# Optimization experiments

Measured on AMD Instinct MI355X. Metric: run time of the kernel, lower is better.

Reference implementation:

```python
import jax, jax.numpy as jnp
import numpy as np

H = 200   # hidden_size
P = 4     # maxout_pool_size
T = 4     # max_dec_steps
B = 64
M = 1000
NEG = -1e30


def setup_inputs():
    key = jax.random.key(0)
    ks = jax.random.split(key, 20)
    def rn(k, shape, scale=0.05):
        return jax.random.normal(k, shape, dtype=jnp.float32) * scale
    inp = {}
    inp["U"] = jax.random.normal(ks[0], (B, M, 2 * H), dtype=jnp.float32)
    inp["d_mask"] = jnp.ones((B, M), dtype=jnp.int32)
    inp["span"] = jax.random.randint(ks[1], (B, 2), 0, M)
    # LSTM: input 4H, hidden H, 1 layer, torch forget-gate bias init (f gate = 1)
    inp["w_ih"] = rn(ks[2], (4 * H, 4 * H))
    inp["w_hh"] = rn(ks[3], (4 * H, H))
    inp["b_ih"] = jnp.zeros((4 * H,), jnp.float32).at[H:2 * H].set(1.0)
    inp["b_hh"] = jnp.zeros((4 * H,), jnp.float32)
    # two HighwayMaxout heads (start 's', end 'e')
    for tag, off in (("s", 4), ("e", 11)):
        inp[f"Wr_{tag}"] = rn(ks[off + 0], (H, 5 * H))          # linear, no bias
        inp[f"W1_{tag}"] = rn(ks[off + 1], (H * P, 3 * H))
        inp[f"b1_{tag}"] = jnp.zeros((H * P,), jnp.float32)
        inp[f"W2_{tag}"] = rn(ks[off + 2], (H * P, H))
        inp[f"b2_{tag}"] = jnp.zeros((H * P,), jnp.float32)
        inp[f"W12_{tag}"] = rn(ks[off + 3], (P, 2 * H))
        inp[f"b12_{tag}"] = jnp.zeros((P,), jnp.float32)
    return inp


def lstm_step(x, h, c, w_ih, w_hh, b_ih, b_hh):
    # torch gate order: i, f, g, o
    g = x @ w_ih.T + h @ w_hh.T + b_ih + b_hh
    i, f, gg, o = jnp.split(g, 4, axis=-1)
    c = jax.nn.sigmoid(f) * c + jax.nn.sigmoid(i) * jnp.tanh(gg)
    h = jax.nn.sigmoid(o) * jnp.tanh(c)
    return h, c


def hmn(h, U, u_cat, mask_mult, Wr, W1, b1, W2, b2, W12, b12):
    b, m, _ = U.shape
    r = jnp.tanh(jnp.concatenate([h, u_cat], 1) @ Wr.T)                      # (b,H)
    x = jnp.concatenate([U, jnp.broadcast_to(r[:, None, :], (b, m, H))], 2)  # (b,m,3H)
    m1 = (x @ W1.T + b1).reshape(b, m, H, P).max(-1)                          # (b,m,H)
    m2 = (m1 @ W2.T + b2).reshape(b, m, H, P).max(-1)                         # (b,m,H)
    alpha = (jnp.concatenate([m1, m2], 2) @ W12.T + b12).max(-1)             # (b,m)
    return jax.nn.log_softmax(alpha + mask_mult, axis=1)


def reference(U, d_mask, span, w_ih, w_hh, b_ih, b_hh,
              Wr_s, W1_s, b1_s, W2_s, b2_s, W12_s, b12_s,
              Wr_e, W1_e, b1_e, W2_e, b2_e, W12_e, b12_e):
    b, m, _ = U.shape
    bidx = jnp.arange(b)
    mask_mult = (1.0 - d_mask.astype(jnp.float32)) * NEG
    s_tgt = span[:, 0]
    e_tgt = span[:, 1]
    ps = (Wr_s, W1_s, b1_s, W2_s, b2_s, W12_s, b12_s)
    pe = (Wr_e, W1_e, b1_e, W2_e, b2_e, W12_e, b12_e)

    s0 = jnp.zeros((b,), jnp.int32)
    e0 = (jnp.sum(d_mask, 1) - 1).astype(jnp.int32)
    u_s0 = U[bidx, s0]
    h0 = jnp.zeros((b, H), U.dtype)
    c0 = jnp.zeros((b, H), U.dtype)
    m0 = jnp.ones((b,), bool)

    def step(carry, first):
        s, e, u_s, h, c, ms, me = carry
        u_e = U[bidx, e]
        u_cat = jnp.concatenate([u_s, u_e], 1)               # (b,4H)
        h, c = lstm_step(u_cat, h, c, w_ih, w_hh, b_ih, b_hh)
        # start head
        a_s = hmn(h, U, u_cat, mask_mult, *ps)
        idx_s = jnp.argmax(a_s, 1).astype(jnp.int32)
        s_new = jnp.where(first, idx_s, idx_s * ms)
        ms_new = jnp.where(first, True, s_new != s * ms)
        ls = -jnp.mean(jnp.take_along_axis(a_s, s_tgt[:, None], 1)) * ms_new.astype(U.dtype)
        # end head (u_s refreshed with new start)
        u_s2 = U[bidx, s_new]
        u_cat2 = jnp.concatenate([u_s2, u_e], 1)
        a_e = hmn(h, U, u_cat2, mask_mult, *pe)
        idx_e = jnp.argmax(a_e, 1).astype(jnp.int32)
        e_new = jnp.where(first, idx_e, idx_e * me)
        me_new = jnp.where(first, True, e_new != e * me)
        le = -jnp.mean(jnp.take_along_axis(a_e, e_tgt[:, None], 1)) * me_new.astype(U.dtype)
        return (s_new, e_new, u_s2, h, c, ms_new, me_new), (s_new, ms_new, e_new, me_new, ls + le)

    firsts = jnp.arange(T) == 0
    _, (ss, mss, es, mes, losses) = jax.lax.scan(step, (s0, e0, u_s0, h0, c0, m0, m0), firsts)

    pos_s = jnp.sum(mss.astype(jnp.int32), 0) - 1            # (b,)
    p1 = ss[pos_s, bidx]
    pos_e = jnp.sum(mes.astype(jnp.int32), 0) - 1
    p2 = es[pos_e, bidx]
    loss = jnp.mean(jnp.sum(losses, 0)) / T
    return loss, p1, p2
```

## Files before the change

### kernel.cpp

```cpp
#include <hip/hip_runtime.h>
#include <math.h>

#define H 200
#define TT 4
#define BB 64
#define MM 1000
#define NEGV (-1e30f)

static const int ROWS = BB * MM;
#define KA 416
#define KB 224
#define NPAD 896
#define NSLICE 28
#define LSTR 40
#define RP 500
#define GG 3528

typedef __attribute__((ext_vector_type(8))) short short8;
typedef __attribute__((ext_vector_type(4))) float f32x4;

__device__ __forceinline__ void split2(float x, unsigned short& h, unsigned short& l) {
  unsigned u = __float_as_uint(x);
  h = (unsigned short)(u >> 16);
  float res = x - __uint_as_float(u & 0xffff0000u);
  l = (unsigned short)(__float_as_uint(res) >> 16);
}
__device__ __forceinline__ float bf2f(unsigned short h) {
  return __uint_as_float(((unsigned)h) << 16);
}
__device__ __forceinline__ void gload16(const unsigned short* g, const unsigned short* l) {
  __builtin_amdgcn_global_load_lds(
      (const __attribute__((address_space(1))) void*)g,
      (__attribute__((address_space(3))) void*)l, 16, 0, 0);
}

__global__ __launch_bounds__(256) void k_init(const int* __restrict__ dmask,
    int* st_s, int* st_e, int* ms, int* me,
    float* h, float* c, float* out) {
  int b = blockIdx.x, t = threadIdx.x;
  __shared__ int red[256];
  int sum = 0;
  for (int m = t; m < MM; m += 256) sum += dmask[b * MM + m];
  red[t] = sum; __syncthreads();
  for (int s = 128; s > 0; s >>= 1) { if (t < s) red[t] += red[t + s]; __syncthreads(); }
  if (t == 0) { st_s[b] = 0; st_e[b] = red[0] - 1; ms[b] = 1; me[b] = 1; }
  for (int i = t; i < H; i += 256) { h[b * H + i] = 0.f; c[b * H + i] = 0.f; }
  if (b == 0 && t == 0) out[0] = 0.f;
}

__global__ __launch_bounds__(256) void k_T(const float* __restrict__ src, int ld,
    int R, int koff, float* __restrict__ dst) {
  int k = blockIdx.x;
  for (int r = threadIdx.x; r < R; r += 256)
    dst[(size_t)k * R + r] = src[(size_t)r * ld + koff + k];
}

__global__ __launch_bounds__(256) void k_splitP(const float* __restrict__ src, int srcld,
    int Ksrc, int Nsrc,
    unsigned short* __restrict__ hi, unsigned short* __restrict__ lo, int Kpad) {
  int r = blockIdx.x;
  int r7 = r & 127;
  size_t pbase = (size_t)(r >> 7) * (size_t)(128 * Kpad);
  int sw = (r7 >> 1) & 3;
  for (int k = threadIdx.x; k < Kpad; k += 256) {
    unsigned short h = 0, l = 0;
    if (r < Nsrc && k < Ksrc) split2(src[(size_t)r * srcld + k], h, l);
    size_t addr = pbase + (size_t)(k >> 5) * 4096 + r7 * 32 +
                  ((((k >> 3) & 3) ^ sw) << 3) + (k & 7);
    hi[addr] = h; lo[addr] = l;
  }
}

__global__ __launch_bounds__(256) void k_splitPW1(const float* __restrict__ src,
    unsigned short* __restrict__ hi, unsigned short* __restrict__ lo) {
  int r = blockIdx.x;
  int o = (r & ~63) + ((r & 15) << 2) + ((r >> 4) & 3);
  int r7 = r & 127;
  size_t pbase = (size_t)(r >> 7) * (size_t)(128 * KA);
  int sw = (r7 >> 1) & 3;
  for (int k = threadIdx.x; k < KA; k += 256) {
    unsigned short h = 0, l = 0;
    if (o < 800 && k < 400) split2(src[(size_t)o * 600 + k], h, l);
    size_t addr = pbase + (size_t)(k >> 5) * 4096 + r7 * 32 +
                  ((((k >> 3) & 3) ^ sw) << 3) + (k & 7);
    hi[addr] = h; lo[addr] = l;
  }
}

__global__ __launch_bounds__(256) void k_split(const float* __restrict__ src, int srcld,
    int Ksrc, int Nsrc,
    unsigned short* __restrict__ hi, unsigned short* __restrict__ lo, int Kpad) {
  int r = blockIdx.x;
  for (int k = threadIdx.x; k < Kpad; k += 256) {
    unsigned short h = 0, l = 0;
    if (r < Nsrc && k < Ksrc) split2(src[(size_t)r * srcld + k], h, l);
    hi[(size_t)r * Kpad + k] = h;
    lo[(size_t)r * Kpad + k] = l;
  }
}

__global__ __launch_bounds__(256) void k_prep(const float* __restrict__ U,
    const int* __restrict__ st_s, const int* __restrict__ st_e,
    float* __restrict__ ucat, float* __restrict__ ue) {
  int b = blockIdx.x, t = threadIdx.x;
  int si = st_s[b], ei = st_e[b];
  const float* Us = U + ((size_t)b * MM + si) * 400;
  const float* Ue = U + ((size_t)b * MM + ei) * 400;
  for (int i = t; i < 400; i += 256) {
    float uv = Ue[i];
    ucat[b * 800 + i] = Us[i];
    ucat[b * 800 + 400 + i] = uv;
    ue[b * 400 + i] = uv;
  }
}

__global__ __launch_bounds__(256) void k_gates(
    const float* __restrict__ ucat, const float* __restrict__ hbuf,
    const float* __restrict__ wTih, const float* __restrict__ wThh,
    const float* __restrict__ b_ih, const float* __restrict__ b_hh,
    float* __restrict__ g) {
  const int b = blockIdx.y, t = threadIdx.x;
  const int o = blockIdx.x * 64 + (t & 63);
  const int oc = o < 800 ? o : 799;
  const int ks = t >> 6;
  __shared__ float xs[800], hs[200], red[256];
  for (int i = t; i < 800; i += 256) xs[i] = ucat[b * 800 + i];
  for (int i = t; i < 200; i += 256) hs[i] = hbuf[b * H + i];
  __syncthreads();
  float acc = 0.f;
#pragma unroll 8
  for (int k = ks * 200; k < ks * 200 + 200; ++k)
    acc = fmaf(wTih[(size_t)k * 800 + oc], xs[k], acc);
#pragma unroll 8
  for (int k = ks * 50; k < ks * 50 + 50; ++k)
    acc = fmaf(wThh[(size_t)k * 800 + oc], hs[k], acc);
  red[t] = acc; __syncthreads();
  if (ks == 0 && o < 800)
    g[b * 800 + o] = red[t] + red[t + 64] + red[t + 128] + red[t + 192] + b_ih[o] + b_hh[o];
}

__global__ __launch_bounds__(256) void k_act(const float* __restrict__ g,
    float* __restrict__ h, float* __restrict__ c) {
  int b = blockIdx.x, t = threadIdx.x;
  if (t >= H) return;
  float ig = 1.f / (1.f + expf(-g[b * 800 + t]));
  float fg = 1.f / (1.f + expf(-g[b * 800 + 200 + t]));
  float gg = tanhf(g[b * 800 + 400 + t]);
  float og = 1.f / (1.f + expf(-g[b * 800 + 600 + t]));
  float cn = fg * c[b * H + t] + ig * gg;
  c[b * H + t] = cn;
  h[b * H + t] = og * tanhf(cn);
}

template <int TAG>
__global__ __launch_bounds__(256) void k_r2(
    const float* __restrict__ U, const int* __restrict__ st_s,
    const float* __restrict__ ucat, const float* __restrict__ ue,
    const float* __restrict__ hbuf, const float* __restrict__ WrT,
    float* __restrict__ rbuf) {
  const int b = blockIdx.y, t = threadIdx.x;
  const int o = blockIdx.x * 64 + (t & 63);
  const int oc = o < 200 ? o : 199;
  const int ks = t >> 6;
  __shared__ float xcs[1000], red[256];
  for (int i = t; i < 200; i += 256) xcs[i] = hbuf[b * H + i];
  if (TAG == 0) {
    for (int i = t; i < 800; i += 256) xcs[200 + i] = ucat[b * 800 + i];
  } else {
    const float* Us = U + ((size_t)b * MM + st_s[b]) * 400;
    for (int i = t; i < 400; i += 256) {
      xcs[200 + i] = Us[i];
      xcs[600 + i] = ue[b * 400 + i];
    }
  }
  __syncthreads();
  float acc = 0.f;
#pragma unroll 8
  for (int k = ks * 250; k < ks * 250 + 250; ++k)
    acc = fmaf(WrT[(size_t)k * 200 + oc], xcs[k], acc);
  red[t] = acc; __syncthreads();
  if (ks == 0 && o < 200)
    rbuf[b * 200 + o] = tanhf(red[t] + red[t + 64] + red[t + 128] + red[t + 192]);
}

__global__ __launch_bounds__(256) void k_rcorr(
    const float* __restrict__ rbuf, const float* __restrict__ W1cT,
    const float* __restrict__ b1, float* __restrict__ rcorr) {
  const int b = blockIdx.y, t = threadIdx.x;
  const int o = blockIdx.x * 64 + (t & 63);
  const int oc = o < 800 ? o : 799;
  const int ks = t >> 6;
  __shared__ float rs[200], red[256];
  for (int i = t; i < 200; i += 256) rs[i] = rbuf[b * 200 + i];
  __syncthreads();
  float acc = 0.f;
#pragma unroll 8
  for (int k = ks * 50; k < ks * 50 + 50; ++k)
    acc = fmaf(W1cT[(size_t)k * 800 + oc], rs[k], acc);
  red[t] = acc; __syncthreads();
  if (ks == 0)
    rcorr[b * NPAD + o] = (o < 800)
        ? red[t] + red[t + 64] + red[t + 128] + red[t + 192] + b1[o] : 0.f;
}

__global__ __launch_bounds__(1024) void k_lstm_r(
    const float* __restrict__ U, const int* __restrict__ st_s, const int* __restrict__ st_e,
    float* __restrict__ h, float* __restrict__ c,
    const float* __restrict__ w_ih, const float* __restrict__ w_hh,
    const float* __restrict__ b_ih, const float* __restrict__ b_hh,
    const float* __restrict__ Wr, const float* __restrict__ W1, const float* __restrict__ b1,
    float* __restrict__ rcorr, float* __restrict__ ue) {
  int b = blockIdx.x, t = threadIdx.x;
  __shared__ float xc[1000];
  __shared__ float hold[H];
  __shared__ float g[800];
  __shared__ float r[H];
  int si = st_s[b], ei = st_e[b];
  const float* Us = U + ((size_t)b * MM + si) * 400;
  const float* Ue = U + ((size_t)b * MM + ei) * 400;
  if (t < 400) { xc[200 + t] = Us[t]; xc[600 + t] = Ue[t]; ue[b * 400 + t] = Ue[t]; }
  if (t >= 400 && t < 600) hold[t - 400] = h[b * H + (t - 400)];
  __syncthreads();
  if (t < 800) {
    float acc = b_ih[t] + b_hh[t];
    const float4* wi = (const float4*)(w_ih + (size_t)t * 800);
    const float* xv = &xc[200];
    for (int k = 0; k < 200; ++k) {
      float4 wv = wi[k];
      acc = fmaf(wv.x, xv[k * 4 + 0], acc); acc = fmaf(wv.y, xv[k * 4 + 1], acc);
      acc = fmaf(wv.z, xv[k * 4 + 2], acc); acc = fmaf(wv.w, xv[k * 4 + 3], acc);
    }
    const float4* wh = (const float4*)(w_hh + (size_t)t * H);
    for (int k = 0; k < 50; ++k) {
      float4 wv = wh[k];
      acc = fmaf(wv.x, hold[k * 4 + 0], acc); acc = fmaf(wv.y, hold[k * 4 + 1], acc);
      acc = fmaf(wv.z, hold[k * 4 + 2], acc); acc = fmaf(wv.w, hold[k * 4 + 3], acc);
    }
    g[t] = acc;
  }
  __syncthreads();
  if (t < H) {
    float ig = 1.f / (1.f + expf(-g[t]));
    float fg = 1.f / (1.f + expf(-g[H + t]));
    float gg = tanhf(g[2 * H + t]);
    float og = 1.f / (1.f + expf(-g[3 * H + t]));
    float cn = fg * c[b * H + t] + ig * gg;
    c[b * H + t] = cn;
    float hv = og * tanhf(cn);
    h[b * H + t] = hv;
    xc[t] = hv;
  }
  __syncthreads();
  if (t < H) {
    float acc = 0.f;
    const float4* wr = (const float4*)(Wr + (size_t)t * 1000);
    for (int k = 0; k < 250; ++k) {
      float4 wv = wr[k];
      acc = fmaf(wv.x, xc[k * 4 + 0], acc); acc = fmaf(wv.y, xc[k * 4 + 1], acc);
      acc = fmaf(wv.z, xc[k * 4 + 2], acc); acc = fmaf(wv.w, xc[k * 4 + 3], acc);
    }
    r[t] = tanhf(acc);
  }
  __syncthreads();
  if (t < NPAD) {
    float acc = 0.f;
    if (t < 800) {
      acc = b1[t];
      const float4* w1 = (const float4*)(W1 + (size_t)t * 600 + 400);
      for (int k = 0; k < 50; ++k) {
        float4 wv = w1[k];
        acc = fmaf(wv.x, r[k * 4 + 0], acc); acc = fmaf(wv.y, r[k * 4 + 1], acc);
        acc = fmaf(wv.z, r[k * 4 + 2], acc); acc = fmaf(wv.w, r[k * 4 + 3], acc);
      }
    }
    rcorr[b * NPAD + t] = acc;
  }
}

__global__ __launch_bounds__(1024) void k_re(
    const float* __restrict__ U, const int* __restrict__ st_s,
    const float* __restrict__ ue, const float* __restrict__ h,
    const float* __restrict__ Wr, const float* __restrict__ W1, const float* __restrict__ b1,
    float* __restrict__ rcorr) {
  int b = blockIdx.x, t = threadIdx.x;
  __shared__ float xc[1000];
  __shared__ float r[H];
  const float* Us = U + ((size_t)b * MM + st_s[b]) * 400;
  if (t < 200) xc[t] = h[b * H + t];
  if (t >= 200 && t < 600) xc[t] = Us[t - 200];
  if (t >= 600 && t < 1000) xc[t] = ue[b * 400 + (t - 600)];
  __syncthreads();
  if (t < H) {
    float acc = 0.f;
    const float4* wr = (const float4*)(Wr + (size_t)t * 1000);
    for (int k = 0; k < 250; ++k) {
      float4 wv = wr[k];
      acc = fmaf(wv.x, xc[k * 4 + 0], acc); acc = fmaf(wv.y, xc[k * 4 + 1], acc);
      acc = fmaf(wv.z, xc[k * 4 + 2], acc); acc = fmaf(wv.w, xc[k * 4 + 3], acc);
    }
    r[t] = tanhf(acc);
  }
  __syncthreads();
  if (t < NPAD) {
    float acc = 0.f;
    if (t < 800) {
      acc = b1[t];
      const float4* w1 = (const float4*)(W1 + (size_t)t * 600 + 400);
      for (int k = 0; k < 50; ++k) {
        float4 wv = w1[k];
        acc = fmaf(wv.x, r[k * 4 + 0], acc); acc = fmaf(wv.y, r[k * 4 + 1], acc);
        acc = fmaf(wv.z, r[k * 4 + 2], acc); acc = fmaf(wv.w, r[k * 4 + 3], acc);
      }
    }
    rcorr[b * NPAD + t] = acc;
  }
}

template <int MODE>
__global__ __launch_bounds__(256, 3) void k_pgemm(
    const unsigned short* __restrict__ Ah, const unsigned short* __restrict__ Al,
    const unsigned short* __restrict__ Bh, const unsigned short* __restrict__ Bl,
    const float* __restrict__ addv,
    unsigned short* __restrict__ Couth, unsigned short* __restrict__ Coutl,
    float* __restrict__ partial, const float* __restrict__ W12) {
  const int Kpad = (MODE == 0) ? KA : KB;
  const int nk = Kpad >> 5;
  __shared__ unsigned short sA[2][8192];
  __shared__ unsigned short sB[8192];
  const int id = blockIdx.x;
  const int g = id / 56, rem = id % 56;
  const int np = rem >> 3, c8 = rem & 7;
  const int rp = g * 8 + c8;
  if (rp >= RP) return;
  const int tid = threadIdx.x;
  const int lane = tid & 63, wave = tid >> 6;
  const int wm = wave >> 1, wn = wave & 1;
  const int row0 = rp * 128, n0 = np * 128;
  const int lr = lane & 15, ls = lane >> 4;
  const size_t panelA = (size_t)rp * (size_t)(128 * Kpad);
  const size_t panelB = (size_t)np * (size_t)(128 * Kpad);
  const int aoff = (wm * 64 + lr) * 32 + ((ls ^ ((lr >> 1) & 3)) << 3);
  const int boff = (wn * 64 + lr) * 32 + ((ls ^ ((lr >> 1) & 3)) << 3);

  f32x4 acc[4][4];
#pragma unroll
  for (int i = 0; i < 4; ++i)
#pragma unroll
    for (int j = 0; j < 4; ++j) acc[i][j] = (f32x4){0.f, 0.f, 0.f, 0.f};

  auto issueA = [&](int buf, int kt) {
    const size_t tA = panelA + (size_t)kt * 4096;
#pragma unroll
    for (int q = 0; q < 2; ++q) {
      const int cc = (q * 4 + wave) * 512;
      gload16(Ah + tA + cc + lane * 8, &sA[buf][cc]);
      gload16(Al + tA + cc + lane * 8, &sA[buf][4096 + cc]);
    }
  };
  auto issueB = [&](int kt) {
    const size_t tB = panelB + (size_t)kt * 4096;
#pragma unroll
    for (int q = 0; q < 2; ++q) {
      const int cc = (q * 4 + wave) * 512;
      gload16(Bh + tB + cc + lane * 8, &sB[cc]);
      gload16(Bl + tB + cc + lane * 8, &sB[4096 + cc]);
    }
  };

  issueA(0, 0);
  issueB(0);
  int cur = 0;
  for (int kt = 0; kt < nk; ++kt) {
    __syncthreads();
    short8 bh[4], bl[4], fah[4], fal[4];
#pragma unroll
    for (int j = 0; j < 4; ++j) {
      bh[j] = *(const short8*)(sB + boff + j * 512);
      bl[j] = *(const short8*)(sB + 4096 + boff + j * 512);
    }
#pragma unroll
    for (int i = 0; i < 4; ++i) {
      fah[i] = *(const short8*)(&sA[cur][0] + aoff + i * 512);
      fal[i] = *(const short8*)(&sA[cur][0] + 4096 + aoff + i * 512);
    }
    __syncthreads();
    if (kt + 1 < nk) { issueA(cur ^ 1, kt + 1); issueB(kt + 1); }
#pragma unroll
    for (int i = 0; i < 4; ++i)
#pragma unroll
      for (int j = 0; j < 4; ++j)
        acc[i][j] = __builtin_amdgcn_mfma_f32_16x16x32_bf16(fah[i], bh[j], acc[i][j], 0, 0, 0);
#pragma unroll
    for (int i = 0; i < 4; ++i)
#pragma unroll
      for (int j = 0; j < 4; ++j)
        acc[i][j] = __builtin_amdgcn_mfma_f32_16x16x32_bf16(fah[i], bl[j], acc[i][j], 0, 0, 0);
#pragma unroll
    for (int i = 0; i < 4; ++i)
#pragma unroll
      for (int j = 0; j < 4; ++j)
        acc[i][j] = __builtin_amdgcn_mfma_f32_16x16x32_bf16(fal[i], bh[j], acc[i][j], 0, 0, 0);
    cur ^= 1;
  }

  if (MODE == 0) {
    const int obase = n0 + wn * 64 + lr * 4;
    const int po = ((n0 + wn * 64) >> 2) + lr;
    const unsigned b0 = (unsigned)row0 / 1000u;
    const unsigned b1 = (unsigned)(row0 + 127) / 1000u;
    float rc0[4], rc1[4];
#pragma unroll
    for (int j = 0; j < 4; ++j) {
      rc0[j] = addv[b0 * NPAD + obase + j];
      rc1[j] = addv[b1 * NPAD + obase + j];
    }
    const size_t panelC = (size_t)rp * (size_t)(128 * KB);
    const size_t addrBase = panelC + (size_t)(po >> 5) * 4096 + (po & 7);
    const int slotb = (po >> 3) & 3;
    const int rowb7 = wm * 64 + ls * 4;
#pragma unroll
    for (int i = 0; i < 4; ++i) {
#pragma unroll
      for (int r = 0; r < 4; ++r) {
        const int r7 = rowb7 + i * 16 + r;
        const int row = row0 + r7;
        const bool useb0 = ((unsigned)row / 1000u) == b0;
        float v = acc[i][0][r] + (useb0 ? rc0[0] : rc1[0]);
        v = fmaxf(v, acc[i][1][r] + (useb0 ? rc0[1] : rc1[1]));
        v = fmaxf(v, acc[i][2][r] + (useb0 ? rc0[2] : rc1[2]));
        v = fmaxf(v, acc[i][3][r] + (useb0 ? rc0[3] : rc1[3]));
        const int sw = (r7 >> 1) & 3;
        size_t addr = addrBase + r7 * 32 + ((slotb ^ sw) << 3);
        unsigned short hh, ll;
        split2(v, hh, ll);
        Couth[addr] = hh;
        Coutl[addr] = ll;
      }
    }
  } else {
    const int colb = n0 + wn * 64 + lr;
    const int rowb7 = wm * 64 + ls * 4;
    const int pmine = lane & 3;
    float w12j[4], addj[4];
#pragma unroll
    for (int j = 0; j < 4; ++j) {
      const int col = colb + j * 16;
      w12j[j] = (col < 800) ? W12[pmine * 400 + 200 + (col >> 2)] : 0.f;
      addj[j] = (col < 800) ? addv[col] : 0.f;
    }
    const int slice = np * 2 + wn;
#pragma unroll
    for (int i = 0; i < 4; ++i) {
#pragma unroll
      for (int r = 0; r < 4; ++r) {
        const int row = row0 + rowb7 + i * 16 + r;
        float sp = 0.f;
#pragma unroll
        for (int j = 0; j < 4; ++j) {
          float v = acc[i][j][r] + addj[j];
          v = fmaxf(v, __shfl_xor(v, 1));
          v = fmaxf(v, __shfl_xor(v, 2));
          sp = fmaf(v, w12j[j], sp);
        }
        sp += __shfl_xor(sp, 4);
        sp += __shfl_xor(sp, 8);
        if (lr < 4)
          partial[((size_t)row * 14 + slice) * 4 + lr] = sp;
      }
    }
  }
}

__global__ __launch_bounds__(256) void k_m1dot(
    const unsigned short* __restrict__ m1h, const unsigned short* __restrict__ m1l,
    const float* __restrict__ partial, const float* __restrict__ W12,
    const float* __restrict__ b12, float* __restrict__ alpha) {
  __shared__ float w12s[4 * 224];
  __shared__ unsigned short th[4096], tl[4096];
  __shared__ float accs[128 * 8];
  const int t = threadIdx.x;
  const int rp = blockIdx.x;
  for (int i = t; i < 896; i += 256) {
    int p = i / 224, k = i - p * 224;
    w12s[i] = (k < 200) ? W12[p * 400 + k] : 0.f;
  }
  const int r7 = t & 127, hhalf = t >> 7;
  const int sw = (r7 >> 1) & 3;
  float a0 = 0.f, a1 = 0.f, a2 = 0.f, a3 = 0.f;
  const size_t panelC = (size_t)rp * (size_t)(128 * KB);
  for (int kt = 0; kt < 7; ++kt) {
    __syncthreads();
    const size_t tb = panelC + (size_t)kt * 4096;
    *(short8*)&th[t * 16] = *(const short8*)(m1h + tb + t * 16);
    *(short8*)&th[t * 16 + 8] = *(const short8*)(m1h + tb + t * 16 + 8);
    *(short8*)&tl[t * 16] = *(const short8*)(m1l + tb + t * 16);
    *(short8*)&tl[t * 16 + 8] = *(const short8*)(m1l + tb + t * 16 + 8);
    __syncthreads();
#pragma unroll
    for (int cc = 0; cc < 2; ++cc) {
      const int c = hhalf * 2 + cc;
      const short8 hv = *(const short8*)&th[r7 * 32 + ((c ^ sw) << 3)];
      const short8 lv = *(const short8*)&tl[r7 * 32 + ((c ^ sw) << 3)];
      const int kb = kt * 32 + c * 8;
#pragma unroll
      for (int e = 0; e < 8; ++e) {
        float val = bf2f((unsigned short)hv[e]) + bf2f((unsigned short)lv[e]);
        const int k = kb + e;
        a0 = fmaf(val, w12s[0 * 224 + k], a0);
        a1 = fmaf(val, w12s[1 * 224 + k], a1);
        a2 = fmaf(val, w12s[2 * 224 + k], a2);
        a3 = fmaf(val, w12s[3 * 224 + k], a3);
      }
    }
  }
  accs[r7 * 8 + hhalf * 4 + 0] = a0;
  accs[r7 * 8 + hhalf * 4 + 1] = a1;
  accs[r7 * 8 + hhalf * 4 + 2] = a2;
  accs[r7 * 8 + hhalf * 4 + 3] = a3;
  __syncthreads();
  if (t < 128) {
    const size_t row = (size_t)rp * 128 + t;
    float4 bb = *(const float4*)b12;
    float s0 = bb.x + accs[t * 8 + 0] + accs[t * 8 + 4];
    float s1 = bb.y + accs[t * 8 + 1] + accs[t * 8 + 5];
    float s2 = bb.z + accs[t * 8 + 2] + accs[t * 8 + 6];
    float s3 = bb.w + accs[t * 8 + 3] + accs[t * 8 + 7];
    const float4* pr = (const float4*)(partial + row * 56);
#pragma unroll
    for (int s = 0; s < 14; ++s) {
      float4 p4 = pr[s];
      s0 += p4.x; s1 += p4.y; s2 += p4.z; s3 += p4.w;
    }
    alpha[row] = fmaxf(fmaxf(s0, s1), fmaxf(s2, s3));
  }
}

__global__ __launch_bounds__(256) void k_argmax(const float* __restrict__ alpha,
    const int* __restrict__ dmask, const int* __restrict__ span, int tag,
    int* __restrict__ idx_out, float* __restrict__ atgt_out) {
  int b = blockIdx.x, t = threadIdx.x;
  __shared__ float vals[MM];
  __shared__ float rv[256];
  __shared__ int ri[256];
  float bestv = -3.4e38f; int besti = 0x7fffffff;
  for (int m = t; m < MM; m += 256) {
    float v = alpha[b * MM + m];
    if (!dmask[b * MM + m]) v += NEGV;
    vals[m] = v;
    if (v > bestv || (v == bestv && m < besti)) { bestv = v; besti = m; }
  }
  rv[t] = bestv; ri[t] = besti; __syncthreads();
  for (int s = 128; s > 0; s >>= 1) {
    if (t < s) {
      float v2 = rv[t + s]; int i2 = ri[t + s];
      if (v2 > rv[t] || (v2 == rv[t] && i2 < ri[t])) { rv[t] = v2; ri[t] = i2; }
    }
    __syncthreads();
  }
  float vmax = rv[0]; int vidx = ri[0];
  __syncthreads();
  float se = 0.f;
  for (int m = t; m < MM; m += 256) se += expf(vals[m] - vmax);
  rv[t] = se; __syncthreads();
  for (int s = 128; s > 0; s >>= 1) { if (t < s) rv[t] += rv[t + s]; __syncthreads(); }
  if (t == 0) {
    int tgt = span[b * 2 + tag];
    atgt_out[b] = vals[tgt] - vmax - logf(rv[0]);
    idx_out[b] = vidx;
  }
}

template <int MODE, int PRESPLIT>
__global__ __launch_bounds__(256) void k_mgemm(
    const float* __restrict__ Af, int lda, int KsrcA,
    const unsigned short* __restrict__ Ah, const unsigned short* __restrict__ Al,
    const unsigned short* __restrict__ Bh, const unsigned short* __restrict__ Bl, int Kpad,
    const float* __restrict__ addv,
    unsigned short* __restrict__ Couth, unsigned short* __restrict__ Coutl,
    float* __restrict__ partial, const float* __restrict__ W12, int slice_base) {
  __shared__ unsigned short sAh[128 * LSTR], sAl[128 * LSTR];
  __shared__ unsigned short sBh[128 * LSTR], sBl[128 * LSTR];
  const int tid = threadIdx.x;
  const int lane = tid & 63, wave = tid >> 6;
  const int wm = wave >> 1, wn = wave & 1;
  const int n0 = blockIdx.x * 128, row0 = blockIdx.y * 128;
  const int lr = lane & 15, ls = lane >> 4;
  f32x4 acc[4][4];
#pragma unroll
  for (int i = 0; i < 4; ++i)
#pragma unroll
    for (int j = 0; j < 4; ++j) acc[i][j] = (f32x4){0.f, 0.f, 0.f, 0.f};
  const int srow = tid >> 1, shalf = tid & 1;
  const float* Afp = Af ? (Af + (size_t)(row0 + srow) * lda + shalf * 16) : nullptr;
  const unsigned short* Ahp = Ah ? (Ah + (size_t)(row0 + srow) * Kpad + shalf * 16) : nullptr;
  const unsigned short* Alp = Al ? (Al + (size_t)(row0 + srow) * Kpad + shalf * 16) : nullptr;
  const unsigned short* Bhp = Bh + (size_t)(n0 + srow) * Kpad + shalf * 16;
  const unsigned short* Blp = Bl + (size_t)(n0 + srow) * Kpad + shalf * 16;
  const int wo = srow * LSTR + shalf * 16;
  const int aoff = (wm * 64 + lr) * LSTR + ls * 8;
  const int boff = (wn * 64 + lr) * LSTR + ls * 8;
  short8 rah0, rah1, ral0, ral1, rbh0, rbh1, rbl0, rbl1;
  auto loadk = [&](int kt) {
    if (PRESPLIT) {
      rah0 = *(const short8*)(Ahp + kt * 32);
      rah1 = *(const short8*)(Ahp + kt * 32 + 8);
      ral0 = *(const short8*)(Alp + kt * 32);
      ral1 = *(const short8*)(Alp + kt * 32 + 8);
    } else {
      const int kk = kt * 32 + shalf * 16;
      float av[16];
#pragma unroll
      for (int q = 0; q < 4; ++q) {
        float4 v;
        if (kk + q * 4 + 4 <= KsrcA) v = *(const float4*)(Afp + kt * 32 + q * 4);
        else v = make_float4(0.f, 0.f, 0.f, 0.f);
        av[q * 4 + 0] = v.x; av[q * 4 + 1] = v.y;
        av[q * 4 + 2] = v.z; av[q * 4 + 3] = v.w;
      }
#pragma unroll
      for (int e = 0; e < 8; ++e) {
        unsigned short hh, ll;
        split2(av[e], hh, ll);     rah0[e] = (short)hh; ral0[e] = (short)ll;
        split2(av[8 + e], hh, ll); rah1[e] = (short)hh; ral1[e] = (short)ll;
      }
    }
    rbh0 = *(const short8*)(Bhp + kt * 32);
    rbh1 = *(const short8*)(Bhp + kt * 32 + 8);
    rbl0 = *(const short8*)(Blp + kt * 32);
    rbl1 = *(const short8*)(Blp + kt * 32 + 8);
  };
  const int nk = Kpad >> 5;
  loadk(0);
  for (int kt = 0; kt < nk; ++kt) {
    *(short8*)&sAh[wo] = rah0; *(short8*)&sAh[wo + 8] = rah1;
    *(short8*)&sAl[wo] = ral0; *(short8*)&sAl[wo + 8] = ral1;
    *(short8*)&sBh[wo] = rbh0; *(short8*)&sBh[wo + 8] = rbh1;
    *(short8*)&sBl[wo] = rbl0; *(short8*)&sBl[wo + 8] = rbl1;
    __syncthreads();
    if (kt + 1 < nk) loadk(kt + 1);
    short8 fa[4], fb[4];
#pragma unroll
    for (int i = 0; i < 4; ++i) fa[i] = *(const short8*)&sAh[aoff + i * 16 * LSTR];
#pragma unroll
    for (int j = 0; j < 4; ++j) fb[j] = *(const short8*)&sBh[boff + j * 16 * LSTR];
#pragma unroll
    for (int i = 0; i < 4; ++i)
#pragma unroll
      for (int j = 0; j < 4; ++j)
        acc[i][j] = __builtin_amdgcn_mfma_f32_16x16x32_bf16(fa[i], fb[j], acc[i][j], 0, 0, 0);
    short8 fc[4];
#pragma unroll
    for (int j = 0; j < 4; ++j) fc[j] = *(const short8*)&sBl[boff + j * 16 * LSTR];
#pragma unroll
    for (int i = 0; i < 4; ++i)
#pragma unroll
      for (int j = 0; j < 4; ++j)
        acc[i][j] = __builtin_amdgcn_mfma_f32_16x16x32_bf16(fa[i], fc[j], acc[i][j], 0, 0, 0);
#pragma unroll
    for (int i = 0; i < 4; ++i) fa[i] = *(const short8*)&sAl[aoff + i * 16 * LSTR];
#pragma unroll
    for (int i = 0; i < 4; ++i)
#pragma unroll
      for (int j = 0; j < 4; ++j)
        acc[i][j] = __builtin_amdgcn_mfma_f32_16x16x32_bf16(fa[i], fb[j], acc[i][j], 0, 0, 0);
    __syncthreads();
  }
  const int colb = n0 + wn * 64 + lr;
  const int rowb = row0 + wm * 64 + ls * 4;
  const int pmine = lane & 3;
  const int woff = (MODE == 0) ? 0 : 200;
  float w12j[4], addj[4];
#pragma unroll
  for (int j = 0; j < 4; ++j) {
    const int col = colb + j * 16;
    w12j[j] = (col < 800) ? W12[pmine * 400 + woff + (col >> 2)] : 0.f;
    if (MODE == 1) addj[j] = (col < 800) ? addv[col] : 0.f;
  }
  const int slice = slice_base + blockIdx.x * 2 + wn;
#pragma unroll
  for (int i = 0; i < 4; ++i) {
#pragma unroll
    for (int r = 0; r < 4; ++r) {
      const int row = rowb + i * 16 + r;
      float sp = 0.f;
#pragma unroll
      for (int j = 0; j < 4; ++j) {
        const int col = colb + j * 16;
        float v = acc[i][j][r];
        if (MODE == 0) {
          const unsigned bidx = (unsigned)row / 1000u;
          v += addv[bidx * NPAD + col];
        } else {
          v += addj[j];
        }
        v = fmaxf(v, __shfl_xor(v, 1));
        v = fmaxf(v, __shfl_xor(v, 2));
        if (MODE == 0 && (lane & 3) == 0) {
          unsigned short hh, ll;
          split2(v, hh, ll);
          Couth[(size_t)row * KB + (col >> 2)] = hh;
          Coutl[(size_t)row * KB + (col >> 2)] = ll;
        }
        sp = fmaf(v, w12j[j], sp);
      }
      sp += __shfl_xor(sp, 4);
      sp += __shfl_xor(sp, 8);
      if (lr < 4)
        partial[((size_t)row * NSLICE + slice) * 4 + lr] = sp;
    }
  }
}

__global__ __launch_bounds__(256) void k_reduce(const float* __restrict__ partial,
    const float* __restrict__ b12, const int* __restrict__ dmask,
    const int* __restrict__ span, int tag,
    int* __restrict__ idx_out, float* __restrict__ atgt_out) {
  int b = blockIdx.x, t = threadIdx.x;
  __shared__ float vals[MM];
  __shared__ float rv[256];
  __shared__ int ri[256];
  float4 bb = *(const float4*)b12;
  float bestv = -3.4e38f; int besti = 0x7fffffff;
  for (int m = t; m < MM; m += 256) {
    const float4* pr = (const float4*)(partial + ((size_t)(b * MM + m)) * (NSLICE * 4));
    float4 a4 = bb;
#pragma unroll
    for (int s = 0; s < NSLICE; ++s) {
      float4 p4 = pr[s];
      a4.x += p4.x; a4.y += p4.y; a4.z += p4.z; a4.w += p4.w;
    }
    float v = fmaxf(fmaxf(a4.x, a4.y), fmaxf(a4.z, a4.w));
    if (!dmask[b * MM + m]) v += NEGV;
    vals[m] = v;
    if (v > bestv || (v == bestv && m < besti)) { bestv = v; besti = m; }
  }
  rv[t] = bestv; ri[t] = besti; __syncthreads();
  for (int s = 128; s > 0; s >>= 1) {
    if (t < s) {
      float v2 = rv[t + s]; int i2 = ri[t + s];
      if (v2 > rv[t] || (v2 == rv[t] && i2 < ri[t])) { rv[t] = v2; ri[t] = i2; }
    }
    __syncthreads();
  }
  float vmax = rv[0]; int vidx = ri[0];
  __syncthreads();
  float se = 0.f;
  for (int m = t; m < MM; m += 256) se += expf(vals[m] - vmax);
  rv[t] = se; __syncthreads();
  for (int s = 128; s > 0; s >>= 1) { if (t < s) rv[t] += rv[t + s]; __syncthreads(); }
  if (t == 0) {
    int tgt = span[b * 2 + tag];
    atgt_out[b] = vals[tgt] - vmax - logf(rv[0]);
    idx_out[b] = vidx;
  }
}

__global__ __launch_bounds__(64) void k_update(const int* __restrict__ idx_buf,
    const float* __restrict__ atgt, int* __restrict__ st, int* __restrict__ mstate,
    float* __restrict__ pout, float* __restrict__ loss, int first) {
  int b = threadIdx.x;
  int idx = idx_buf[b];
  int sold = st[b], msold = mstate[b];
  int snew = first ? idx : (msold ? idx : 0);
  int msnew = first ? 1 : ((snew != (msold ? sold : 0)) ? 1 : 0);
  st[b] = snew; mstate[b] = msnew;
  if (msnew) pout[b] = (float)snew;
  float asum = atgt[b];
  float csum = (float)msnew;
  for (int off = 32; off > 0; off >>= 1) {
    asum += __shfl_down(asum, off);
    csum += __shfl_down(csum, off);
  }
  if (b == 0) loss[0] += (-asum / (float)BB) * csum / (float)(BB * TT);
}

extern "C" void kernel_launch(void* const* d_in, const int* in_sizes, int n_in,
                              void* d_out, int out_size, void* d_ws, size_t ws_size,
                              hipStream_t stream) {
  const float* U     = (const float*)d_in[0];
  const int*   dmask = (const int*)d_in[1];
  const int*   span  = (const int*)d_in[2];
  const float* w_ih  = (const float*)d_in[3];
  const float* w_hh  = (const float*)d_in[4];
  const float* b_ih  = (const float*)d_in[5];
  const float* b_hh  = (const float*)d_in[6];
  const float* Wr[2]  = {(const float*)d_in[7],  (const float*)d_in[14]};
  const float* W1[2]  = {(const float*)d_in[8],  (const float*)d_in[15]};
  const float* b1[2]  = {(const float*)d_in[9],  (const float*)d_in[16]};
  const float* W2[2]  = {(const float*)d_in[10], (const float*)d_in[17]};
  const float* b2[2]  = {(const float*)d_in[11], (const float*)d_in[18]};
  const float* W12[2] = {(const float*)d_in[12], (const float*)d_in[19]};
  const float* b12[2] = {(const float*)d_in[13], (const float*)d_in[20]};
  float* out = (float*)d_out;

  size_t off = 0;
  char* base = (char*)d_ws;
  auto alloc = [&](size_t n) {
    void* p = base + off;
    off += (n + 255) & ~(size_t)255;
    return p;
  };
  float* rcorr = (float*)alloc((size_t)BB * NPAD * 4);
  float* ue    = (float*)alloc((size_t)BB * 400 * 4);
  float* ucat  = (float*)alloc((size_t)BB * 800 * 4);
  float* gbuf  = (float*)alloc((size_t)BB * 800 * 4);
  float* rbuf  = (float*)alloc((size_t)BB * 200 * 4);
  float* hbuf  = (float*)alloc((size_t)BB * H * 4);
  float* cbuf  = (float*)alloc((size_t)BB * H * 4);
  float* alphab = (float*)alloc((size_t)ROWS * 4);
  float* atgt  = (float*)alloc((size_t)BB * 4);
  int* st_s = (int*)alloc(BB * 4);
  int* st_e = (int*)alloc(BB * 4);
  int* msb  = (int*)alloc(BB * 4);
  int* meb  = (int*)alloc(BB * 4);
  int* idxb = (int*)alloc(BB * 4);
  unsigned short *W1h[2], *W1l[2], *W2h[2], *W2l[2];
  for (int g = 0; g < 2; ++g) {
    W1h[g] = (unsigned short*)alloc((size_t)NPAD * KA * 2);
    W1l[g] = (unsigned short*)alloc((size_t)NPAD * KA * 2);
    W2h[g] = (unsigned short*)alloc((size_t)NPAD * KB * 2);
    W2l[g] = (unsigned short*)alloc((size_t)NPAD * KB * 2);
  }
  unsigned short* m1h = (unsigned short*)alloc((size_t)ROWS * KB * 2);
  unsigned short* m1l = (unsigned short*)alloc((size_t)ROWS * KB * 2);

  const size_t P14_B  = (size_t)ROWS * 14 * 4 * 4;
  const size_t TIH_B  = (size_t)800 * 800 * 4;
  const size_t THH_B  = (size_t)200 * 800 * 4;
  const size_t TWR_B  = (size_t)1000 * 200 * 4;
  const size_t TW1_B  = (size_t)200 * 800 * 4;
  const size_t UHL_B  = (size_t)ROWS * KA * 2;
  size_t panel_need = off + P14_B + TIH_B + THH_B + 2 * TWR_B + 2 * TW1_B + 2 * UHL_B + 4096;
  bool panelPath = (ws_size >= panel_need);

  if (panelPath) {
    float* partial = (float*)alloc(P14_B);
    float* wTih = (float*)alloc(TIH_B);
    float* wThh = (float*)alloc(THH_B);
    float* WrT[2]  = {(float*)alloc(TWR_B), (float*)alloc(TWR_B)};
    float* W1cT[2] = {(float*)alloc(TW1_B), (float*)alloc(TW1_B)};
    unsigned short* Uh = (unsigned short*)alloc(UHL_B);
    unsigned short* Ul = (unsigned short*)alloc(UHL_B);

    k_init<<<BB, 256, 0, stream>>>(dmask, st_s, st_e, msb, meb, hbuf, cbuf, out);
    for (int g = 0; g < 2; ++g) {
      k_splitPW1<<<NPAD, 256, 0, stream>>>(W1[g], W1h[g], W1l[g]);
      k_splitP<<<NPAD, 256, 0, stream>>>(W2[g], 200, 200, 800, W2h[g], W2l[g], KB);
      k_T<<<1000, 256, 0, stream>>>(Wr[g], 1000, 200, 0, WrT[g]);
      k_T<<<200, 256, 0, stream>>>(W1[g], 600, 800, 400, W1cT[g]);
    }
    k_T<<<800, 256, 0, stream>>>(w_ih, 800, 800, 0, wTih);
    k_T<<<200, 256, 0, stream>>>(w_hh, 200, 800, 0, wThh);
    k_splitP<<<ROWS, 256, 0, stream>>>(U, 400, 400, ROWS, Uh, Ul, KA);

    dim3 g13(13, BB), g4(4, BB), g14(14, BB);
    for (int t = 0; t < TT; ++t) {
      int first = (t == 0) ? 1 : 0;
      k_prep<<<BB, 256, 0, stream>>>(U, st_s, st_e, ucat, ue);
      k_gates<<<g13, 256, 0, stream>>>(ucat, hbuf, wTih, wThh, b_ih, b_hh, gbuf);
      k_act<<<BB, 256, 0, stream>>>(gbuf, hbuf, cbuf);
      k_r2<0><<<g4, 256, 0, stream>>>(U, st_s, ucat, ue, hbuf, WrT[0], rbuf);
      k_rcorr<<<g14, 256, 0, stream>>>(rbuf, W1cT[0], b1[0], rcorr);
      k_pgemm<0><<<GG, 256, 0, stream>>>(Uh, Ul, W1h[0], W1l[0],
          rcorr, m1h, m1l, nullptr, nullptr);
      k_pgemm<1><<<GG, 256, 0, stream>>>(m1h, m1l, W2h[0], W2l[0],
          b2[0], nullptr, nullptr, partial, W12[0]);
      k_m1dot<<<RP, 256, 0, stream>>>(m1h, m1l, partial, W12[0], b12[0], alphab);
      k_argmax<<<BB, 256, 0, stream>>>(alphab, dmask, span, 0, idxb, atgt);
      k_update<<<1, 64, 0, stream>>>(idxb, atgt, st_s, msb, out + 1, out, first);
      k_r2<1><<<g4, 256, 0, stream>>>(U, st_s, ucat, ue, hbuf, WrT[1], rbuf);
      k_rcorr<<<g14, 256, 0, stream>>>(rbuf, W1cT[1], b1[1], rcorr);
      k_pgemm<0><<<GG, 256, 0, stream>>>(Uh, Ul, W1h[1], W1l[1],
          rcorr, m1h, m1l, nullptr, nullptr);
      k_pgemm<1><<<GG, 256, 0, stream>>>(m1h, m1l, W2h[1], W2l[1],
          b2[1], nullptr, nullptr, partial, W12[1]);
      k_m1dot<<<RP, 256, 0, stream>>>(m1h, m1l, partial, W12[1], b12[1], alphab);
      k_argmax<<<BB, 256, 0, stream>>>(alphab, dmask, span, 1, idxb, atgt);
      k_update<<<1, 64, 0, stream>>>(idxb, atgt, st_e, meb, out + 1 + BB, out, first);
    }
  } else {
    float* partial = (float*)alloc((size_t)ROWS * NSLICE * 4 * 4);
    k_init<<<BB, 256, 0, stream>>>(dmask, st_s, st_e, msb, meb, hbuf, cbuf, out);
    for (int g = 0; g < 2; ++g) {
      k_split<<<NPAD, 256, 0, stream>>>(W1[g], 600, 400, 800, W1h[g], W1l[g], KA);
      k_split<<<NPAD, 256, 0, stream>>>(W2[g], 200, 200, 800, W2h[g], W2l[g], KB);
    }
    dim3 gg(NPAD / 128, ROWS / 128);
    for (int t = 0; t < TT; ++t) {
      int first = (t == 0) ? 1 : 0;
      for (int tag = 0; tag < 2; ++tag) {
        if (tag == 0)
          k_lstm_r<<<BB, 1024, 0, stream>>>(U, st_s, st_e, hbuf, cbuf, w_ih, w_hh, b_ih, b_hh,
                                            Wr[0], W1[0], b1[0], rcorr, ue);
        else
          k_re<<<BB, 1024, 0, stream>>>(U, st_s, ue, hbuf, Wr[1], W1[1], b1[1], rcorr);

        k_mgemm<0, 0><<<gg, 256, 0, stream>>>(U, 400, 400, nullptr, nullptr,
            W1h[tag], W1l[tag], KA, rcorr, m1h, m1l, partial, W12[tag], 0);
        k_mgemm<1, 1><<<gg, 256, 0, stream>>>(nullptr, 0, 0, m1h, m1l,
            W2h[tag], W2l[tag], KB, b2[tag], nullptr, nullptr, partial, W12[tag], 14);

        k_reduce<<<BB, 256, 0, stream>>>(partial, b12[tag], dmask, span, tag, idxb, atgt);
        if (tag == 0)
          k_update<<<1, 64, 0, stream>>>(idxb, atgt, st_s, msb, out + 1, out, first);
        else
          k_update<<<1, 64, 0, stream>>>(idxb, atgt, st_e, meb, out + 1 + BB, out, first);
      }
    }
  }
}
```

Before: 2.063 ms.

## Fuse m1·W12 dot into second GEMM and partial reduction into argmax

Removes the separate k_m1dot kernel. One of the seven N-panel blocks per row panel of the MODE 1 GEMM computes the m1·W12 dot product from the A tiles it already holds in shared memory, and the partial-sum reduction plus max over pools moves into k_argmax. This saves a launch and a re-read of m1 from global memory per head step. In exchange, the chosen blocks do extra ALU work inside the GEMM loop, which can imbalance them, and the W12 load into shared memory adds setup to every MODE 1 block.

```diff
diff --git a/kernel.cpp b/kernel.cpp
--- a/kernel.cpp
+++ b/kernel.cpp
@@ -322,11 +322,13 @@
     const unsigned short* __restrict__ Bh, const unsigned short* __restrict__ Bl,
     const float* __restrict__ addv,
     unsigned short* __restrict__ Couth, unsigned short* __restrict__ Coutl,
-    float* __restrict__ partial, const float* __restrict__ W12) {
+    float* __restrict__ partial, const float* __restrict__ W12,
+    float* __restrict__ m1w12) {
   const int Kpad = (MODE == 0) ? KA : KB;
   const int nk = Kpad >> 5;
   __shared__ unsigned short sA[2][8192];
   __shared__ unsigned short sB[8192];
+  __shared__ float w12s[(MODE == 1) ? 896 : 4];
   const int id = blockIdx.x;
   const int g = id / 56, rem = id % 56;
   const int np = rem >> 3, c8 = rem & 7;
@@ -341,12 +343,21 @@
   const size_t panelB = (size_t)np * (size_t)(128 * Kpad);
   const int aoff = (wm * 64 + lr) * 32 + ((ls ^ ((lr >> 1) & 3)) << 3);
   const int boff = (wn * 64 + lr) * 32 + ((ls ^ ((lr >> 1) & 3)) << 3);
+  const bool doDot = (MODE == 1) && (np == rp % 7);
+
+  if (MODE == 1) {
+    for (int i = tid; i < 896; i += 256) {
+      int p = i / 224, k = i - p * 224;
+      w12s[i] = (k < 200) ? W12[p * 400 + k] : 0.f;
+    }
+  }
 
   f32x4 acc[4][4];
 #pragma unroll
   for (int i = 0; i < 4; ++i)
 #pragma unroll
     for (int j = 0; j < 4; ++j) acc[i][j] = (f32x4){0.f, 0.f, 0.f, 0.f};
+  float d0 = 0.f, d1 = 0.f, d2 = 0.f, d3 = 0.f;
 
   auto issueA = [&](int buf, int kt) {
     const size_t tA = panelA + (size_t)kt * 4096;
@@ -383,6 +394,27 @@
       fah[i] = *(const short8*)(&sA[cur][0] + aoff + i * 512);
       fal[i] = *(const short8*)(&sA[cur][0] + 4096 + aoff + i * 512);
     }
+    if (doDot) {
+      const int r7d = tid >> 1, kh = tid & 1;
+      const int swd = (r7d >> 1) & 3;
+      const int base = r7d * 32;
+      const int kb = kt * 32 + kh * 16;
+#pragma unroll
+      for (int gq = 0; gq < 2; ++gq) {
+        const int slot = kh * 2 + gq;
+        const short8 hv = *(const short8*)(&sA[cur][0] + base + ((slot ^ swd) << 3));
+        const short8 lv = *(const short8*)(&sA[cur][0] + 4096 + base + ((slot ^ swd) << 3));
+#pragma unroll
+        for (int e = 0; e < 8; ++e) {
+          float val = bf2f((unsigned short)hv[e]) + bf2f((unsigned short)lv[e]);
+          const int k = kb + gq * 8 + e;
+          d0 = fmaf(val, w12s[k], d0);
+          d1 = fmaf(val, w12s[224 + k], d1);
+          d2 = fmaf(val, w12s[448 + k], d2);
+          d3 = fmaf(val, w12s[672 + k], d3);
+        }
+      }
+    }
     __syncthreads();
     if (kt + 1 < nk) { issueA(cur ^ 1, kt + 1); issueB(kt + 1); }
 #pragma unroll
@@ -401,6 +433,15 @@
       for (int j = 0; j < 4; ++j)
         acc[i][j] = __builtin_amdgcn_mfma_f32_16x16x32_bf16(fal[i], bh[j], acc[i][j], 0, 0, 0);
     cur ^= 1;
+  }
+
+  if (doDot) {
+    d0 += __shfl_xor(d0, 1); d1 += __shfl_xor(d1, 1);
+    d2 += __shfl_xor(d2, 1); d3 += __shfl_xor(d3, 1);
+    if ((tid & 1) == 0) {
+      const int row = row0 + (tid >> 1);
+      *(float4*)(m1w12 + (size_t)row * 4) = make_float4(d0, d1, d2, d3);
+    }
   }
 
   if (MODE == 0) {
@@ -471,80 +512,28 @@
   }
 }
 
-__global__ __launch_bounds__(256) void k_m1dot(
-    const unsigned short* __restrict__ m1h, const unsigned short* __restrict__ m1l,
-    const float* __restrict__ partial, const float* __restrict__ W12,
-    const float* __restrict__ b12, float* __restrict__ alpha) {
-  __shared__ float w12s[4 * 224];
-  __shared__ unsigned short th[4096], tl[4096];
-  __shared__ float accs[128 * 8];
-  const int t = threadIdx.x;
-  const int rp = blockIdx.x;
-  for (int i = t; i < 896; i += 256) {
-    int p = i / 224, k = i - p * 224;
-    w12s[i] = (k < 200) ? W12[p * 400 + k] : 0.f;
-  }
-  const int r7 = t & 127, hhalf = t >> 7;
-  const int sw = (r7 >> 1) & 3;
-  float a0 = 0.f, a1 = 0.f, a2 = 0.f, a3 = 0.f;
-  const size_t panelC = (size_t)rp * (size_t)(128 * KB);
-  for (int kt = 0; kt < 7; ++kt) {
-    __syncthreads();
-    const size_t tb = panelC + (size_t)kt * 4096;
-    *(short8*)&th[t * 16] = *(const short8*)(m1h + tb + t * 16);
-    *(short8*)&th[t * 16 + 8] = *(const short8*)(m1h + tb + t * 16 + 8);
-    *(short8*)&tl[t * 16] = *(const short8*)(m1l + tb + t * 16);
-    *(short8*)&tl[t * 16 + 8] = *(const short8*)(m1l + tb + t * 16 + 8);
-    __syncthreads();
-#pragma unroll
-    for (int cc = 0; cc < 2; ++cc) {
-      const int c = hhalf * 2 + cc;
-      const short8 hv = *(const short8*)&th[r7 * 32 + ((c ^ sw) << 3)];
-      const short8 lv = *(const short8*)&tl[r7 * 32 + ((c ^ sw) << 3)];
-      const int kb = kt * 32 + c * 8;
-#pragma unroll
-      for (int e = 0; e < 8; ++e) {
-        float val = bf2f((unsigned short)hv[e]) + bf2f((unsigned short)lv[e]);
-        const int k = kb + e;
-        a0 = fmaf(val, w12s[0 * 224 + k], a0);
-        a1 = fmaf(val, w12s[1 * 224 + k], a1);
-        a2 = fmaf(val, w12s[2 * 224 + k], a2);
-        a3 = fmaf(val, w12s[3 * 224 + k], a3);
-      }
-    }
-  }
-  accs[r7 * 8 + hhalf * 4 + 0] = a0;
-  accs[r7 * 8 + hhalf * 4 + 1] = a1;
-  accs[r7 * 8 + hhalf * 4 + 2] = a2;
-  accs[r7 * 8 + hhalf * 4 + 3] = a3;
-  __syncthreads();
-  if (t < 128) {
-    const size_t row = (size_t)rp * 128 + t;
-    float4 bb = *(const float4*)b12;
-    float s0 = bb.x + accs[t * 8 + 0] + accs[t * 8 + 4];
-    float s1 = bb.y + accs[t * 8 + 1] + accs[t * 8 + 5];
-    float s2 = bb.z + accs[t * 8 + 2] + accs[t * 8 + 6];
-    float s3 = bb.w + accs[t * 8 + 3] + accs[t * 8 + 7];
-    const float4* pr = (const float4*)(partial + row * 56);
-#pragma unroll
-    for (int s = 0; s < 14; ++s) {
-      float4 p4 = pr[s];
-      s0 += p4.x; s1 += p4.y; s2 += p4.z; s3 += p4.w;
-    }
-    alpha[row] = fmaxf(fmaxf(s0, s1), fmaxf(s2, s3));
-  }
-}
-
-__global__ __launch_bounds__(256) void k_argmax(const float* __restrict__ alpha,
-    const int* __restrict__ dmask, const int* __restrict__ span, int tag,
+__global__ __launch_bounds__(256) void k_argmax(
+    const float* __restrict__ partial, const float* __restrict__ m1w12,
+    const float* __restrict__ b12, const int* __restrict__ dmask,
+    const int* __restrict__ span, int tag,
     int* __restrict__ idx_out, float* __restrict__ atgt_out) {
   int b = blockIdx.x, t = threadIdx.x;
   __shared__ float vals[MM];
   __shared__ float rv[256];
   __shared__ int ri[256];
+  float4 bb = *(const float4*)b12;
   float bestv = -3.4e38f; int besti = 0x7fffffff;
   for (int m = t; m < MM; m += 256) {
-    float v = alpha[b * MM + m];
+    const size_t row = (size_t)b * MM + m;
+    float4 a4 = *(const float4*)(m1w12 + row * 4);
+    a4.x += bb.x; a4.y += bb.y; a4.z += bb.z; a4.w += bb.w;
+    const float4* pr = (const float4*)(partial + row * 56);
+#pragma unroll
+    for (int s = 0; s < 14; ++s) {
+      float4 p4 = pr[s];
+      a4.x += p4.x; a4.y += p4.y; a4.z += p4.z; a4.w += p4.w;
+    }
+    float v = fmaxf(fmaxf(a4.x, a4.y), fmaxf(a4.z, a4.w));
     if (!dmask[b * MM + m]) v += NEGV;
     vals[m] = v;
     if (v > bestv || (v == bestv && m < besti)) { bestv = v; besti = m; }
@@ -807,7 +796,7 @@
   float* rbuf  = (float*)alloc((size_t)BB * 200 * 4);
   float* hbuf  = (float*)alloc((size_t)BB * H * 4);
   float* cbuf  = (float*)alloc((size_t)BB * H * 4);
-  float* alphab = (float*)alloc((size_t)ROWS * 4);
+  float* m1w12 = (float*)alloc((size_t)ROWS * 4 * 4);
   float* atgt  = (float*)alloc((size_t)BB * 4);
   int* st_s = (int*)alloc(BB * 4);
   int* st_e = (int*)alloc(BB * 4);
@@ -862,20 +851,18 @@
       k_r2<0><<<g4, 256, 0, stream>>>(U, st_s, ucat, ue, hbuf, WrT[0], rbuf);
       k_rcorr<<<g14, 256, 0, stream>>>(rbuf, W1cT[0], b1[0], rcorr);
       k_pgemm<0><<<GG, 256, 0, stream>>>(Uh, Ul, W1h[0], W1l[0],
-          rcorr, m1h, m1l, nullptr, nullptr);
+          rcorr, m1h, m1l, nullptr, nullptr, nullptr);
       k_pgemm<1><<<GG, 256, 0, stream>>>(m1h, m1l, W2h[0], W2l[0],
-          b2[0], nullptr, nullptr, partial, W12[0]);
-      k_m1dot<<<RP, 256, 0, stream>>>(m1h, m1l, partial, W12[0], b12[0], alphab);
-      k_argmax<<<BB, 256, 0, stream>>>(alphab, dmask, span, 0, idxb, atgt);
+          b2[0], nullptr, nullptr, partial, W12[0], m1w12);
+      k_argmax<<<BB, 256, 0, stream>>>(partial, m1w12, b12[0], dmask, span, 0, idxb, atgt);
       k_update<<<1, 64, 0, stream>>>(idxb, atgt, st_s, msb, out + 1, out, first);
       k_r2<1><<<g4, 256, 0, stream>>>(U, st_s, ucat, ue, hbuf, WrT[1], rbuf);
       k_rcorr<<<g14, 256, 0, stream>>>(rbuf, W1cT[1], b1[1], rcorr);
       k_pgemm<0><<<GG, 256, 0, stream>>>(Uh, Ul, W1h[1], W1l[1],
-          rcorr, m1h, m1l, nullptr, nullptr);
+          rcorr, m1h, m1l, nullptr, nullptr, nullptr);
       k_pgemm<1><<<GG, 256, 0, stream>>>(m1h, m1l, W2h[1], W2l[1],
-          b2[1], nullptr, nullptr, partial, W12[1]);
-      k_m1dot<<<RP, 256, 0, stream>>>(m1h, m1l, partial, W12[1], b12[1], alphab);
-      k_argmax<<<BB, 256, 0, stream>>>(alphab, dmask, span, 1, idxb, atgt);
+          b2[1], nullptr, nullptr, partial, W12[1], m1w12);
+      k_argmax<<<BB, 256, 0, stream>>>(partial, m1w12, b12[1], dmask, span, 1, idxb, atgt);
       k_update<<<1, 64, 0, stream>>>(idxb, atgt, st_e, meb, out + 1 + BB, out, first);
     }
   } else {
```

After: 2.216 ms. 1.07x slower.
